# Performance work log

Hardware: AMD Instinct MI355X
Metric: run time of the kernel (lower is better)

The kernel has to match this reference:

```python
import jax, jax.numpy as jnp
import numpy as np

N_NODES = 50000
N_EDGES = 800000
IN_CH, HID_CH, OUT_CH = 128, 128, 64


def setup_inputs() -> dict:
    key = jax.random.key(0)
    k1, k2, k3, k4, k5, k6 = jax.random.split(key, 6)
    x = jax.random.normal(k1, (N_NODES, IN_CH), dtype=jnp.float32)
    edge_index = jax.random.randint(k2, (2, N_EDGES), 0, N_NODES, dtype=jnp.int64)
    # Glorot init like PyG GCNConv; bias zeros-like but random small for test coverage
    s1 = jnp.sqrt(6.0 / (IN_CH + HID_CH)).astype(jnp.float32)
    s2 = jnp.sqrt(6.0 / (HID_CH + OUT_CH)).astype(jnp.float32)
    W1 = jax.random.uniform(k3, (IN_CH, HID_CH), jnp.float32, -s1, s1)
    b1 = jax.random.normal(k4, (HID_CH,), jnp.float32) * 0.01
    W2 = jax.random.uniform(k5, (HID_CH, OUT_CH), jnp.float32, -s2, s2)
    b2 = jax.random.normal(k6, (OUT_CH,), jnp.float32) * 0.01
    return {"x": x, "edge_index": edge_index, "W1": W1, "b1": b1, "W2": W2, "b2": b2}


def gcn_conv(x, edge_index, W, b):
    """PyG GCNConv: add self-loops, symmetric D^-1/2 (A+I) D^-1/2 normalization,
    then aggregate linearly-transformed neighbor features + bias."""
    n = x.shape[0]
    h = x @ W  # [N, F_out]
    src, dst = edge_index[0], edge_index[1]
    # degree counts self-loop (weight 1) plus in-edges at dst
    deg = 1.0 + jax.ops.segment_sum(jnp.ones_like(src, dtype=h.dtype), dst, num_segments=n)
    dinv = jax.lax.rsqrt(deg)  # deg >= 1, no zeros
    norm = dinv[src] * dinv[dst]  # [E]
    agg = jax.ops.segment_sum(h[src] * norm[:, None], dst, num_segments=n)
    # self-loop contribution: norm = dinv[i]*dinv[i] = 1/deg[i]
    return agg + h * (1.0 / deg)[:, None] + b


def reference(x, edge_index, W1, b1, W2, b2):
    # eval-mode forward: dropout is identity
    h = gcn_conv(x, edge_index, W1, b1)
    h = jax.nn.relu(h)
    out = gcn_conv(h, edge_index, W2, b2)
    return out
```

## Files before the change

### kernel.cpp

```cpp
#include <hip/hip_runtime.h>
#include <hip/hip_fp16.h>


typedef _Float16 f16;
typedef __attribute__((ext_vector_type(8))) _Float16 f16x8;
typedef __attribute__((ext_vector_type(4))) float f32x4;

__global__ __launch_bounds__(256) void deg_prep_kernel(const int* __restrict__ dst,
                                                       int* __restrict__ deg,
                                                       int* __restrict__ posw,
                                                       const float* __restrict__ W1,
                                                       const float* __restrict__ W2,
                                                       f16* __restrict__ Wt1,
                                                       f16* __restrict__ Wt2, int E) {
    int gid = blockIdx.x * 256 + threadIdx.x;
    if (gid < E) posw[gid] = atomicAdd(&deg[dst[gid]], 1);
    if (gid < 128 * 128) {
        int k = gid >> 7, c = gid & 127;
        Wt1[c * 136 + k] = (f16)W1[gid];
    } else if (gid < 128 * 128 + 128 * 64) {
        int j = gid - 128 * 128;
        int k = j >> 6, c = j & 63;
        Wt2[c * 136 + k] = (f16)W2[j];
    }
}

__global__ __launch_bounds__(1024) void scan1_kernel(const int* __restrict__ deg,
                                                     int* __restrict__ rowptr,
                                                     int* __restrict__ bsum,
                                                     float* __restrict__ dinv, int N) {
    __shared__ int wsum[16];
    const int tid = threadIdx.x, lane = tid & 63, wid = tid >> 6;
    const int idx = blockIdx.x * 1024 + tid;
    int v = (idx < N) ? deg[idx] : 0;
    if (idx < N) dinv[idx] = rsqrtf((float)v + 1.0f);
    int incl = v;
#pragma unroll
    for (int off = 1; off < 64; off <<= 1) {
        int t = __shfl_up(incl, off, 64);
        if (lane >= off) incl += t;
    }
    if (lane == 63) wsum[wid] = incl;
    __syncthreads();
    if (wid == 0) {
        int s = (lane < 16) ? wsum[lane] : 0;
#pragma unroll
        for (int off = 1; off < 16; off <<= 1) {
            int t = __shfl_up(s, off, 64);
            if (lane >= off) s += t;
        }
        if (lane < 16) wsum[lane] = s;
    }
    __syncthreads();
    int waveoff = (wid == 0) ? 0 : wsum[wid - 1];
    if (idx < N) rowptr[idx] = waveoff + incl - v;
    if (tid == 1023) bsum[blockIdx.x] = waveoff + incl;
}

__global__ __launch_bounds__(1024) void scan23_kernel(int* __restrict__ rowptr,
                                                      const int* __restrict__ bsum,
                                                      int N, int nb) {
    __shared__ int pfx_s;
    const int tid = threadIdx.x;
    if (tid < 64) {
        int v = (tid < nb && tid < blockIdx.x) ? bsum[tid] : 0;
#pragma unroll
        for (int off = 32; off; off >>= 1) v += __shfl_xor(v, off, 64);
        if (tid == 0) pfx_s = v;
    }
    if (blockIdx.x == 0 && tid >= 64 && tid < 128) {
        int l = tid - 64;
        int v = (l < nb) ? bsum[l] : 0;
#pragma unroll
        for (int off = 32; off; off >>= 1) v += __shfl_xor(v, off, 64);
        if (l == 0) rowptr[N] = v;
    }
    __syncthreads();
    int idx = blockIdx.x * 1024 + tid;
    if (idx < N) rowptr[idx] += pfx_s;
}

template <int KOUT, bool F32IN>
__device__ __forceinline__ void gemm_body(int bid, const void* __restrict__ Xv,
                                          const f16* __restrict__ Wt,
                                          f16* __restrict__ H, int N, f16* Wl) {
    constexpr int CT = KOUT / 16;
    const int tid = threadIdx.x;
    constexpr int CHUNKS = KOUT * 136 / 8;
    {
        const uint4* s = (const uint4*)Wt;
        uint4* d = (uint4*)Wl;
        for (int i = tid; i < CHUNKS; i += 256) d[i] = s[i];
    }
    __syncthreads();

    const int lane = tid & 63, wid = tid >> 6;
    const int c = lane & 15, kseg = lane >> 4;
    const int row0 = bid * 64 + wid * 16;
    int arow = row0 + c;
    if (arow >= N) arow = N - 1;

    f32x4 acc[CT];
#pragma unroll
    for (int t = 0; t < CT; ++t) acc[t] = (f32x4){0.f, 0.f, 0.f, 0.f};

#pragma unroll
    for (int kt = 0; kt < 4; ++kt) {
        const int k0 = kt * 32;
        f16x8 a;
        if (F32IN) {
            const float* xp = (const float*)Xv + (long)arow * 128 + k0 + kseg * 8;
            float4 x0 = *(const float4*)xp;
            float4 x1 = *(const float4*)(xp + 4);
            a[0] = (f16)x0.x; a[1] = (f16)x0.y; a[2] = (f16)x0.z; a[3] = (f16)x0.w;
            a[4] = (f16)x1.x; a[5] = (f16)x1.y; a[6] = (f16)x1.z; a[7] = (f16)x1.w;
        } else {
            a = *(const f16x8*)((const f16*)Xv + (long)arow * 128 + k0 + kseg * 8);
        }
#pragma unroll
        for (int ct = 0; ct < CT; ++ct) {
            f16x8 b = *(const f16x8*)&Wl[(ct * 16 + c) * 136 + k0 + kseg * 8];
            acc[ct] = __builtin_amdgcn_mfma_f32_16x16x32_f16(a, b, acc[ct], 0, 0, 0);
        }
    }

    const int rbase = row0 + kseg * 4;
#pragma unroll
    for (int ct = 0; ct < CT; ++ct)
#pragma unroll
        for (int r = 0; r < 4; ++r) {
            int row = rbase + r;
            if (row < N) H[(long)row * KOUT + ct * 16 + c] = (f16)acc[ct][r];
        }
}

template <int KOUT, bool F32IN>
__global__ __launch_bounds__(256) void gemm_kernel(const void* __restrict__ Xv,
                                                   const f16* __restrict__ Wt,
                                                   f16* __restrict__ H, int N) {
    __shared__ f16 Wl[KOUT * 136];
    gemm_body<KOUT, F32IN>(blockIdx.x, Xv, Wt, H, N, Wl);
}

__global__ __launch_bounds__(256) void fill_gemm_kernel(const int* __restrict__ src,
                                                        const int* __restrict__ dst,
                                                        const int* __restrict__ posw,
                                                        const float* __restrict__ dinv,
                                                        const int* __restrict__ rowptr,
                                                        float2* __restrict__ pairs, int E,
                                                        const float* __restrict__ x,
                                                        const f16* __restrict__ Wt1,
                                                        f16* __restrict__ h1, int N, int GB) {
    __shared__ f16 Wl[128 * 136];
    if ((int)blockIdx.x < GB) {
        gemm_body<128, true>(blockIdx.x, x, Wt1, h1, N, Wl);
        return;
    }
    int e = (blockIdx.x - GB) * 256 + threadIdx.x;
    if (e >= E) return;
    int s = src[e], d = dst[e];
    float2 p;
    p.x = __int_as_float(s);
    p.y = dinv[s] * dinv[d];
    pairs[rowptr[d] + posw[e]] = p;
}

template <int F, bool RELU, bool OUTF16>
__global__ __launch_bounds__(256) void gather_kernel(const void* __restrict__ Hv,
                                                     const int* __restrict__ rowptr,
                                                     const float2* __restrict__ pairs,
                                                     const float* __restrict__ dinv,
                                                     const float* __restrict__ bias,
                                                     void* __restrict__ outv, int N) {
    const int wid = threadIdx.x >> 6;
    const int lane = threadIdx.x & 63;
    const int node = blockIdx.x * 4 + wid;
    if (node >= N) return;
    const int start = rowptr[node], end = rowptr[node + 1];
    const float4* pp4 = (const float4*)pairs;

    if (F == 128) {
        const __half2* Hu = (const __half2*)Hv;
        float ax = 0.f, ay = 0.f;
        int e = start;
        if ((e & 1) && e < end) {
            float2 p0 = pairs[e];
            float2 f0 = __half22float2(Hu[(long)__float_as_int(p0.x) * 64 + lane]);
            ax += f0.x * p0.y; ay += f0.y * p0.y;
            ++e;
        }
        for (; e + 15 < end; e += 16) {
            float4 q[8];
#pragma unroll
            for (int j = 0; j < 8; ++j) q[j] = pp4[(e >> 1) + j];
            __half2 uu[16];
#pragma unroll
            for (int j = 0; j < 8; ++j) {
                uu[2 * j]     = Hu[(long)__float_as_int(q[j].x) * 64 + lane];
                uu[2 * j + 1] = Hu[(long)__float_as_int(q[j].z) * 64 + lane];
            }
#pragma unroll
            for (int j = 0; j < 8; ++j) {
                float2 f0 = __half22float2(uu[2 * j]);
                float2 f1 = __half22float2(uu[2 * j + 1]);
                ax += f0.x * q[j].y + f1.x * q[j].w;
                ay += f0.y * q[j].y + f1.y * q[j].w;
            }
        }
        for (; e + 3 < end; e += 4) {
            float4 q0 = pp4[e >> 1], q1 = pp4[(e >> 1) + 1];
            __half2 u0 = Hu[(long)__float_as_int(q0.x) * 64 + lane];
            __half2 u1 = Hu[(long)__float_as_int(q0.z) * 64 + lane];
            __half2 u2 = Hu[(long)__float_as_int(q1.x) * 64 + lane];
            __half2 u3 = Hu[(long)__float_as_int(q1.z) * 64 + lane];
            float2 f0 = __half22float2(u0), f1 = __half22float2(u1);
            float2 f2 = __half22float2(u2), f3 = __half22float2(u3);
            ax += f0.x * q0.y + f1.x * q0.w + f2.x * q1.y + f3.x * q1.w;
            ay += f0.y * q0.y + f1.y * q0.w + f2.y * q1.y + f3.y * q1.w;
        }
        for (; e < end; ++e) {
            float2 p0 = pairs[e];
            float2 f0 = __half22float2(Hu[(long)__float_as_int(p0.x) * 64 + lane]);
            ax += f0.x * p0.y; ay += f0.y * p0.y;
        }
        float di = dinv[node];
        float d2 = di * di;
        float2 fs = __half22float2(Hu[(long)node * 64 + lane]);
        float2 bz = ((const float2*)bias)[lane];
        float zx = ax + fs.x * d2 + bz.x;
        float zy = ay + fs.y * d2 + bz.y;
        if (RELU) { zx = fmaxf(zx, 0.f); zy = fmaxf(zy, 0.f); }
        if (OUTF16) {
            ((__half2*)outv)[(long)node * 64 + lane] = __float22half2_rn(make_float2(zx, zy));
        } else {
            float2 o = {zx, zy};
            ((float2*)outv)[(long)node * 64 + lane] = o;
        }
    } else {
        const __half* Hh = (const __half*)Hv;
        float acc = 0.f;
        int e = start;
        if ((e & 1) && e < end) {
            float2 p0 = pairs[e];
            acc += __half2float(Hh[(long)__float_as_int(p0.x) * 64 + lane]) * p0.y;
            ++e;
        }
        for (; e + 15 < end; e += 16) {
            float4 q[8];
#pragma unroll
            for (int j = 0; j < 8; ++j) q[j] = pp4[(e >> 1) + j];
            __half uu[16];
#pragma unroll
            for (int j = 0; j < 8; ++j) {
                uu[2 * j]     = Hh[(long)__float_as_int(q[j].x) * 64 + lane];
                uu[2 * j + 1] = Hh[(long)__float_as_int(q[j].z) * 64 + lane];
            }
#pragma unroll
            for (int j = 0; j < 8; ++j)
                acc += __half2float(uu[2 * j]) * q[j].y + __half2float(uu[2 * j + 1]) * q[j].w;
        }
        for (; e + 3 < end; e += 4) {
            float4 q0 = pp4[e >> 1], q1 = pp4[(e >> 1) + 1];
            float h0 = __half2float(Hh[(long)__float_as_int(q0.x) * 64 + lane]);
            float h1 = __half2float(Hh[(long)__float_as_int(q0.z) * 64 + lane]);
            float h2 = __half2float(Hh[(long)__float_as_int(q1.x) * 64 + lane]);
            float h3 = __half2float(Hh[(long)__float_as_int(q1.z) * 64 + lane]);
            acc += h0 * q0.y + h1 * q0.w + h2 * q1.y + h3 * q1.w;
        }
        for (; e < end; ++e) {
            float2 p0 = pairs[e];
            acc += __half2float(Hh[(long)__float_as_int(p0.x) * 64 + lane]) * p0.y;
        }
        float di = dinv[node];
        float z = acc + __half2float(Hh[(long)node * 64 + lane]) * (di * di) + bias[lane];
        if (RELU) z = fmaxf(z, 0.f);
        ((float*)outv)[(long)node * 64 + lane] = z;
    }
}

extern "C" void kernel_launch(void* const* d_in, const int* in_sizes, int n_in,
                              void* d_out, int out_size, void* d_ws, size_t ws_size,
                              hipStream_t stream) {
    const float* x  = (const float*)d_in[0];
    const int*   ei = (const int*)d_in[1];
    const float* W1 = (const float*)d_in[2];
    const float* b1 = (const float*)d_in[3];
    const float* W2 = (const float*)d_in[4];
    const float* b2 = (const float*)d_in[5];
    float* out = (float*)d_out;

    const int N = in_sizes[0] / 128;
    const int E = in_sizes[1] / 2;
    const int* src = ei;
    const int* dst = ei + E;
    const int NB = (N + 1023) / 1024;

    float* ws = (float*)d_ws;
    float2* pairs = (float2*)ws;
    long off = 2L * E;
    int* posw   = (int*)(ws + off); off += E;
    int* deg    = (int*)(ws + off); off += N;
    int* rowptr = (int*)(ws + off); off += N + 1;
    int* bsum   = (int*)(ws + off); off += 64;
    float* dinv = ws + off;        off += N;
    off = (off + 3) & ~3L;
    f16* Wt1 = (f16*)(ws + off); off += (128 * 136) / 2;
    f16* Wt2 = (f16*)(ws + off); off += (64 * 136) / 2;
    f16* h1  = (f16*)(ws + off); off += (long)N * 64;
    f16* z1  = (f16*)(ws + off); off += (long)N * 64;
    f16* h2  = (f16*)(ws + off); off += (long)N * 32;

    hipMemsetAsync(deg, 0, (size_t)N * sizeof(int), stream);
    deg_prep_kernel<<<(E + 255) / 256, 256, 0, stream>>>(dst, deg, posw, W1, W2, Wt1, Wt2, E);
    scan1_kernel<<<NB, 1024, 0, stream>>>(deg, rowptr, bsum, dinv, N);
    scan23_kernel<<<NB, 1024, 0, stream>>>(rowptr, bsum, N, NB);

    const int GB = (N + 63) / 64;
    const int FB = (E + 255) / 256;
    fill_gemm_kernel<<<GB + FB, 256, 0, stream>>>(src, dst, posw, dinv, rowptr, pairs, E,
                                                  x, Wt1, h1, N, GB);

    gather_kernel<128, true, true><<<(N + 3) / 4, 256, 0, stream>>>(h1, rowptr, pairs, dinv, b1, z1, N);

    gemm_kernel<64, false><<<(N + 63) / 64, 256, 0, stream>>>(z1, Wt2, h2, N);
    gather_kernel<64, false, false><<<(N + 3) / 4, 256, 0, stream>>>(h2, rowptr, pairs, dinv, b2, out, N);
}
```

Before: 228.7 us.

## Fuse degree counting with first GEMM and split layer-1 gather into column halves

The separate weight-transpose pass is removed, and each GEMM block now converts the fp32 weights to transposed fp16 in shared memory itself. The degree atomics are fused into the first GEMM launch, so the GEMM runs before the scan instead of alongside the fill. Fill becomes its own kernel. The 128-wide first-layer gather is split into two launches, each covering 64 columns with one half per lane, which may improve cache locality of each pass but reads the CSR pairs twice and adds launches. Every GEMM block now redoes the weight conversion, which adds redundant work.

```diff
diff --git a/kernel.cpp b/kernel.cpp
--- a/kernel.cpp
+++ b/kernel.cpp
@@ -5,25 +5,6 @@
 typedef _Float16 f16;
 typedef __attribute__((ext_vector_type(8))) _Float16 f16x8;
 typedef __attribute__((ext_vector_type(4))) float f32x4;
-
-__global__ __launch_bounds__(256) void deg_prep_kernel(const int* __restrict__ dst,
-                                                       int* __restrict__ deg,
-                                                       int* __restrict__ posw,
-                                                       const float* __restrict__ W1,
-                                                       const float* __restrict__ W2,
-                                                       f16* __restrict__ Wt1,
-                                                       f16* __restrict__ Wt2, int E) {
-    int gid = blockIdx.x * 256 + threadIdx.x;
-    if (gid < E) posw[gid] = atomicAdd(&deg[dst[gid]], 1);
-    if (gid < 128 * 128) {
-        int k = gid >> 7, c = gid & 127;
-        Wt1[c * 136 + k] = (f16)W1[gid];
-    } else if (gid < 128 * 128 + 128 * 64) {
-        int j = gid - 128 * 128;
-        int k = j >> 6, c = j & 63;
-        Wt2[c * 136 + k] = (f16)W2[j];
-    }
-}
 
 __global__ __launch_bounds__(1024) void scan1_kernel(const int* __restrict__ deg,
                                                      int* __restrict__ rowptr,
@@ -80,17 +61,35 @@
     if (idx < N) rowptr[idx] += pfx_s;
 }
 
+__global__ __launch_bounds__(256) void fill_kernel(const int* __restrict__ src,
+                                                   const int* __restrict__ dst,
+                                                   const int* __restrict__ posw,
+                                                   const float* __restrict__ dinv,
+                                                   const int* __restrict__ rowptr,
+                                                   float2* __restrict__ pairs, int E) {
+    int e = blockIdx.x * 256 + threadIdx.x;
+    if (e >= E) return;
+    int s = src[e], d = dst[e];
+    float2 p;
+    p.x = __int_as_float(s);
+    p.y = dinv[s] * dinv[d];
+    pairs[rowptr[d] + posw[e]] = p;
+}
+
 template <int KOUT, bool F32IN>
 __device__ __forceinline__ void gemm_body(int bid, const void* __restrict__ Xv,
-                                          const f16* __restrict__ Wt,
+                                          const float* __restrict__ W,
                                           f16* __restrict__ H, int N, f16* Wl) {
     constexpr int CT = KOUT / 16;
     const int tid = threadIdx.x;
-    constexpr int CHUNKS = KOUT * 136 / 8;
-    {
-        const uint4* s = (const uint4*)Wt;
-        uint4* d = (uint4*)Wl;
-        for (int i = tid; i < CHUNKS; i += 256) d[i] = s[i];
+    for (int i4 = tid; i4 < 128 * KOUT / 4; i4 += 256) {
+        int flat = i4 * 4;
+        int k = flat / KOUT, c = flat % KOUT;
+        float4 w = *(const float4*)&W[flat];
+        Wl[(c + 0) * 136 + k] = (f16)w.x;
+        Wl[(c + 1) * 136 + k] = (f16)w.y;
+        Wl[(c + 2) * 136 + k] = (f16)w.z;
+        Wl[(c + 3) * 136 + k] = (f16)w.w;
     }
     __syncthreads();
 
@@ -136,37 +135,29 @@
 
 template <int KOUT, bool F32IN>
 __global__ __launch_bounds__(256) void gemm_kernel(const void* __restrict__ Xv,
-                                                   const f16* __restrict__ Wt,
+                                                   const float* __restrict__ W,
                                                    f16* __restrict__ H, int N) {
     __shared__ f16 Wl[KOUT * 136];
-    gemm_body<KOUT, F32IN>(blockIdx.x, Xv, Wt, H, N, Wl);
-}
-
-__global__ __launch_bounds__(256) void fill_gemm_kernel(const int* __restrict__ src,
-                                                        const int* __restrict__ dst,
-                                                        const int* __restrict__ posw,
-                                                        const float* __restrict__ dinv,
-                                                        const int* __restrict__ rowptr,
-                                                        float2* __restrict__ pairs, int E,
-                                                        const float* __restrict__ x,
-                                                        const f16* __restrict__ Wt1,
-                                                        f16* __restrict__ h1, int N, int GB) {
+    gemm_body<KOUT, F32IN>(blockIdx.x, Xv, W, H, N, Wl);
+}
+
+__global__ __launch_bounds__(256) void deg_gemm_kernel(const int* __restrict__ dst,
+                                                       int* __restrict__ deg,
+                                                       int* __restrict__ posw, int E,
+                                                       const float* __restrict__ x,
+                                                       const float* __restrict__ W1,
+                                                       f16* __restrict__ h1, int N, int GB) {
     __shared__ f16 Wl[128 * 136];
     if ((int)blockIdx.x < GB) {
-        gemm_body<128, true>(blockIdx.x, x, Wt1, h1, N, Wl);
+        gemm_body<128, true>(blockIdx.x, x, W1, h1, N, Wl);
         return;
     }
     int e = (blockIdx.x - GB) * 256 + threadIdx.x;
-    if (e >= E) return;
-    int s = src[e], d = dst[e];
-    float2 p;
-    p.x = __int_as_float(s);
-    p.y = dinv[s] * dinv[d];
-    pairs[rowptr[d] + posw[e]] = p;
-}
-
-template <int F, bool RELU, bool OUTF16>
-__global__ __launch_bounds__(256) void gather_kernel(const void* __restrict__ Hv,
+    if (e < E) posw[e] = atomicAdd(&deg[dst[e]], 1);
+}
+
+template <int STRIDE, int COLOFF, bool RELU, bool OUTF16>
+__global__ __launch_bounds__(256) void gather_kernel(const __half* __restrict__ H,
                                                      const int* __restrict__ rowptr,
                                                      const float2* __restrict__ pairs,
                                                      const float* __restrict__ dinv,
@@ -178,103 +169,48 @@
     if (node >= N) return;
     const int start = rowptr[node], end = rowptr[node + 1];
     const float4* pp4 = (const float4*)pairs;
-
-    if (F == 128) {
-        const __half2* Hu = (const __half2*)Hv;
-        float ax = 0.f, ay = 0.f;
-        int e = start;
-        if ((e & 1) && e < end) {
-            float2 p0 = pairs[e];
-            float2 f0 = __half22float2(Hu[(long)__float_as_int(p0.x) * 64 + lane]);
-            ax += f0.x * p0.y; ay += f0.y * p0.y;
-            ++e;
-        }
-        for (; e + 15 < end; e += 16) {
-            float4 q[8];
-#pragma unroll
-            for (int j = 0; j < 8; ++j) q[j] = pp4[(e >> 1) + j];
-            __half2 uu[16];
-#pragma unroll
-            for (int j = 0; j < 8; ++j) {
-                uu[2 * j]     = Hu[(long)__float_as_int(q[j].x) * 64 + lane];
-                uu[2 * j + 1] = Hu[(long)__float_as_int(q[j].z) * 64 + lane];
-            }
-#pragma unroll
-            for (int j = 0; j < 8; ++j) {
-                float2 f0 = __half22float2(uu[2 * j]);
-                float2 f1 = __half22float2(uu[2 * j + 1]);
-                ax += f0.x * q[j].y + f1.x * q[j].w;
-                ay += f0.y * q[j].y + f1.y * q[j].w;
-            }
-        }
-        for (; e + 3 < end; e += 4) {
-            float4 q0 = pp4[e >> 1], q1 = pp4[(e >> 1) + 1];
-            __half2 u0 = Hu[(long)__float_as_int(q0.x) * 64 + lane];
-            __half2 u1 = Hu[(long)__float_as_int(q0.z) * 64 + lane];
-            __half2 u2 = Hu[(long)__float_as_int(q1.x) * 64 + lane];
-            __half2 u3 = Hu[(long)__float_as_int(q1.z) * 64 + lane];
-            float2 f0 = __half22float2(u0), f1 = __half22float2(u1);
-            float2 f2 = __half22float2(u2), f3 = __half22float2(u3);
-            ax += f0.x * q0.y + f1.x * q0.w + f2.x * q1.y + f3.x * q1.w;
-            ay += f0.y * q0.y + f1.y * q0.w + f2.y * q1.y + f3.y * q1.w;
-        }
-        for (; e < end; ++e) {
-            float2 p0 = pairs[e];
-            float2 f0 = __half22float2(Hu[(long)__float_as_int(p0.x) * 64 + lane]);
-            ax += f0.x * p0.y; ay += f0.y * p0.y;
-        }
-        float di = dinv[node];
-        float d2 = di * di;
-        float2 fs = __half22float2(Hu[(long)node * 64 + lane]);
-        float2 bz = ((const float2*)bias)[lane];
-        float zx = ax + fs.x * d2 + bz.x;
-        float zy = ay + fs.y * d2 + bz.y;
-        if (RELU) { zx = fmaxf(zx, 0.f); zy = fmaxf(zy, 0.f); }
-        if (OUTF16) {
-            ((__half2*)outv)[(long)node * 64 + lane] = __float22half2_rn(make_float2(zx, zy));
-        } else {
-            float2 o = {zx, zy};
-            ((float2*)outv)[(long)node * 64 + lane] = o;
-        }
+    const __half* Hh = H + COLOFF + lane;
+
+    float acc = 0.f;
+    int e = start;
+    if ((e & 1) && e < end) {
+        float2 p0 = pairs[e];
+        acc += __half2float(Hh[(long)__float_as_int(p0.x) * STRIDE]) * p0.y;
+        ++e;
+    }
+    for (; e + 15 < end; e += 16) {
+        float4 q[8];
+#pragma unroll
+        for (int j = 0; j < 8; ++j) q[j] = pp4[(e >> 1) + j];
+        __half uu[16];
+#pragma unroll
+        for (int j = 0; j < 8; ++j) {
+            uu[2 * j]     = Hh[(long)__float_as_int(q[j].x) * STRIDE];
+            uu[2 * j + 1] = Hh[(long)__float_as_int(q[j].z) * STRIDE];
+        }
+#pragma unroll
+        for (int j = 0; j < 8; ++j)
+            acc += __half2float(uu[2 * j]) * q[j].y + __half2float(uu[2 * j + 1]) * q[j].w;
+    }
+    for (; e + 3 < end; e += 4) {
+        float4 q0 = pp4[e >> 1], q1 = pp4[(e >> 1) + 1];
+        float h0 = __half2float(Hh[(long)__float_as_int(q0.x) * STRIDE]);
+        float h1 = __half2float(Hh[(long)__float_as_int(q0.z) * STRIDE]);
+        float h2 = __half2float(Hh[(long)__float_as_int(q1.x) * STRIDE]);
+        float h3 = __half2float(Hh[(long)__float_as_int(q1.z) * STRIDE]);
+        acc += h0 * q0.y + h1 * q0.w + h2 * q1.y + h3 * q1.w;
+    }
+    for (; e < end; ++e) {
+        float2 p0 = pairs[e];
+        acc += __half2float(Hh[(long)__float_as_int(p0.x) * STRIDE]) * p0.y;
+    }
+    float di = dinv[node];
+    float z = acc + __half2float(Hh[(long)node * STRIDE]) * (di * di) + bias[COLOFF + lane];
+    if (RELU) z = fmaxf(z, 0.f);
+    if (OUTF16) {
+        ((__half*)outv)[(long)node * STRIDE + COLOFF + lane] = __float2half(z);
     } else {
-        const __half* Hh = (const __half*)Hv;
-        float acc = 0.f;
-        int e = start;
-        if ((e & 1) && e < end) {
-            float2 p0 = pairs[e];
-            acc += __half2float(Hh[(long)__float_as_int(p0.x) * 64 + lane]) * p0.y;
-            ++e;
-        }
-        for (; e + 15 < end; e += 16) {
-            float4 q[8];
-#pragma unroll
-            for (int j = 0; j < 8; ++j) q[j] = pp4[(e >> 1) + j];
-            __half uu[16];
-#pragma unroll
-            for (int j = 0; j < 8; ++j) {
-                uu[2 * j]     = Hh[(long)__float_as_int(q[j].x) * 64 + lane];
-                uu[2 * j + 1] = Hh[(long)__float_as_int(q[j].z) * 64 + lane];
-            }
-#pragma unroll
-            for (int j = 0; j < 8; ++j)
-                acc += __half2float(uu[2 * j]) * q[j].y + __half2float(uu[2 * j + 1]) * q[j].w;
-        }
-        for (; e + 3 < end; e += 4) {
-            float4 q0 = pp4[e >> 1], q1 = pp4[(e >> 1) + 1];
-            float h0 = __half2float(Hh[(long)__float_as_int(q0.x) * 64 + lane]);
-            float h1 = __half2float(Hh[(long)__float_as_int(q0.z) * 64 + lane]);
-            float h2 = __half2float(Hh[(long)__float_as_int(q1.x) * 64 + lane]);
-            float h3 = __half2float(Hh[(long)__float_as_int(q1.z) * 64 + lane]);
-            acc += h0 * q0.y + h1 * q0.w + h2 * q1.y + h3 * q1.w;
-        }
-        for (; e < end; ++e) {
-            float2 p0 = pairs[e];
-            acc += __half2float(Hh[(long)__float_as_int(p0.x) * 64 + lane]) * p0.y;
-        }
-        float di = dinv[node];
-        float z = acc + __half2float(Hh[(long)node * 64 + lane]) * (di * di) + bias[lane];
-        if (RELU) z = fmaxf(z, 0.f);
-        ((float*)outv)[(long)node * 64 + lane] = z;
+        ((float*)outv)[(long)node * STRIDE + COLOFF + lane] = z;
     }
 }
 
@@ -304,24 +240,25 @@
     int* bsum   = (int*)(ws + off); off += 64;
     float* dinv = ws + off;        off += N;
     off = (off + 3) & ~3L;
-    f16* Wt1 = (f16*)(ws + off); off += (128 * 136) / 2;
-    f16* Wt2 = (f16*)(ws + off); off += (64 * 136) / 2;
-    f16* h1  = (f16*)(ws + off); off += (long)N * 64;
-    f16* z1  = (f16*)(ws + off); off += (long)N * 64;
-    f16* h2  = (f16*)(ws + off); off += (long)N * 32;
+    f16* h1 = (f16*)(ws + off); off += (long)N * 64;
+    f16* z1 = (f16*)(ws + off); off += (long)N * 64;
+    f16* h2 = (f16*)(ws + off); off += (long)N * 32;
+
+    const int GB = (N + 63) / 64;
+    const int DB = (E + 255) / 256;
 
     hipMemsetAsync(deg, 0, (size_t)N * sizeof(int), stream);
-    deg_prep_kernel<<<(E + 255) / 256, 256, 0, stream>>>(dst, deg, posw, W1, W2, Wt1, Wt2, E);
+    deg_gemm_kernel<<<GB + DB, 256, 0, stream>>>(dst, deg, posw, E, x, W1, h1, N, GB);
     scan1_kernel<<<NB, 1024, 0, stream>>>(deg, rowptr, bsum, dinv, N);
     scan23_kernel<<<NB, 1024, 0, stream>>>(rowptr, bsum, N, NB);
-
-    const int GB = (N + 63) / 64;
-    const int FB = (E + 255) / 256;
-    fill_gemm_kernel<<<GB + FB, 256, 0, stream>>>(src, dst, posw, dinv, rowptr, pairs, E,
-                                                  x, Wt1, h1, N, GB);
-
-    gather_kernel<128, true, true><<<(N + 3) / 4, 256, 0, stream>>>(h1, rowptr, pairs, dinv, b1, z1, N);
-
-    gemm_kernel<64, false><<<(N + 63) / 64, 256, 0, stream>>>(z1, Wt2, h2, N);
-    gather_kernel<64, false, false><<<(N + 3) / 4, 256, 0, stream>>>(h2, rowptr, pairs, dinv, b2, out, N);
-}
+    fill_kernel<<<(E + 255) / 256, 256, 0, stream>>>(src, dst, posw, dinv, rowptr, pairs, E);
+
+    gather_kernel<128, 0, true, true><<<(N + 3) / 4, 256, 0, stream>>>(
+        (const __half*)h1, rowptr, pairs, dinv, b1, z1, N);
+    gather_kernel<128, 64, true, true><<<(N + 3) / 4, 256, 0, stream>>>(
+        (const __half*)h1, rowptr, pairs, dinv, b1, z1, N);
+
+    gemm_kernel<64, false><<<(N + 63) / 64, 256, 0, stream>>>(z1, W2, h2, N);
+    gather_kernel<64, 0, false, false><<<(N + 3) / 4, 256, 0, stream>>>(
+        (const __half*)h2, rowptr, pairs, dinv, b2, out, N);
+}
```

Result: slower. 253.1 us (+10.7%).

## Fuse layer-1 aggregation with per-node layer-2 GEMV and drop weight prep

Applied to the files above, without the earlier changes.

The layer-1 gather now also performs the ReLU and multiplies the node's hidden row by W2 in LDS. This removes the z1 intermediate buffer and the separate second GEMM launch. Weight transposition to fp16 moves into each GEMM and gather block, read straight from the fp32 weights, so the standalone weight-prep work is gone. The cost is that every 4-node gather block re-reads and transposes the whole 32KB W2 into LDS. That adds a large amount of redundant L2 traffic, LDS stores that may hit bank conflicts, and higher LDS use that can limit occupancy.

```diff
diff --git a/kernel.cpp b/kernel.cpp
--- a/kernel.cpp
+++ b/kernel.cpp
@@ -6,23 +6,11 @@
 typedef __attribute__((ext_vector_type(8))) _Float16 f16x8;
 typedef __attribute__((ext_vector_type(4))) float f32x4;
 
-__global__ __launch_bounds__(256) void deg_prep_kernel(const int* __restrict__ dst,
-                                                       int* __restrict__ deg,
-                                                       int* __restrict__ posw,
-                                                       const float* __restrict__ W1,
-                                                       const float* __restrict__ W2,
-                                                       f16* __restrict__ Wt1,
-                                                       f16* __restrict__ Wt2, int E) {
-    int gid = blockIdx.x * 256 + threadIdx.x;
-    if (gid < E) posw[gid] = atomicAdd(&deg[dst[gid]], 1);
-    if (gid < 128 * 128) {
-        int k = gid >> 7, c = gid & 127;
-        Wt1[c * 136 + k] = (f16)W1[gid];
-    } else if (gid < 128 * 128 + 128 * 64) {
-        int j = gid - 128 * 128;
-        int k = j >> 6, c = j & 63;
-        Wt2[c * 136 + k] = (f16)W2[j];
-    }
+__global__ __launch_bounds__(256) void deg_pos_kernel(const int* __restrict__ dst,
+                                                      int* __restrict__ deg,
+                                                      int* __restrict__ posw, int E) {
+    int e = blockIdx.x * 256 + threadIdx.x;
+    if (e < E) posw[e] = atomicAdd(&deg[dst[e]], 1);
 }
 
 __global__ __launch_bounds__(1024) void scan1_kernel(const int* __restrict__ deg,
@@ -82,15 +70,18 @@
 
 template <int KOUT, bool F32IN>
 __device__ __forceinline__ void gemm_body(int bid, const void* __restrict__ Xv,
-                                          const f16* __restrict__ Wt,
+                                          const float* __restrict__ W,
                                           f16* __restrict__ H, int N, f16* Wl) {
     constexpr int CT = KOUT / 16;
     const int tid = threadIdx.x;
-    constexpr int CHUNKS = KOUT * 136 / 8;
-    {
-        const uint4* s = (const uint4*)Wt;
-        uint4* d = (uint4*)Wl;
-        for (int i = tid; i < CHUNKS; i += 256) d[i] = s[i];
+    for (int i4 = tid; i4 < 128 * KOUT / 4; i4 += 256) {
+        int flat = i4 * 4;
+        int k = flat / KOUT, c = flat % KOUT;
+        float4 w = *(const float4*)&W[flat];
+        Wl[(c + 0) * 136 + k] = (f16)w.x;
+        Wl[(c + 1) * 136 + k] = (f16)w.y;
+        Wl[(c + 2) * 136 + k] = (f16)w.z;
+        Wl[(c + 3) * 136 + k] = (f16)w.w;
     }
     __syncthreads();
 
@@ -134,14 +125,6 @@
         }
 }
 
-template <int KOUT, bool F32IN>
-__global__ __launch_bounds__(256) void gemm_kernel(const void* __restrict__ Xv,
-                                                   const f16* __restrict__ Wt,
-                                                   f16* __restrict__ H, int N) {
-    __shared__ f16 Wl[KOUT * 136];
-    gemm_body<KOUT, F32IN>(blockIdx.x, Xv, Wt, H, N, Wl);
-}
-
 __global__ __launch_bounds__(256) void fill_gemm_kernel(const int* __restrict__ src,
                                                         const int* __restrict__ dst,
                                                         const int* __restrict__ posw,
@@ -149,11 +132,11 @@
                                                         const int* __restrict__ rowptr,
                                                         float2* __restrict__ pairs, int E,
                                                         const float* __restrict__ x,
-                                                        const f16* __restrict__ Wt1,
+                                                        const float* __restrict__ W1,
                                                         f16* __restrict__ h1, int N, int GB) {
     __shared__ f16 Wl[128 * 136];
     if ((int)blockIdx.x < GB) {
-        gemm_body<128, true>(blockIdx.x, x, Wt1, h1, N, Wl);
+        gemm_body<128, true>(blockIdx.x, x, W1, h1, N, Wl);
         return;
     }
     int e = (blockIdx.x - GB) * 256 + threadIdx.x;
@@ -165,13 +148,103 @@
     pairs[rowptr[d] + posw[e]] = p;
 }
 
-template <int F, bool RELU, bool OUTF16>
-__global__ __launch_bounds__(256) void gather_kernel(const void* __restrict__ Hv,
-                                                     const int* __restrict__ rowptr,
-                                                     const float2* __restrict__ pairs,
-                                                     const float* __restrict__ dinv,
-                                                     const float* __restrict__ bias,
-                                                     void* __restrict__ outv, int N) {
+__global__ __launch_bounds__(256) void gather_gemv_kernel(const __half* __restrict__ H,
+                                                          const int* __restrict__ rowptr,
+                                                          const float2* __restrict__ pairs,
+                                                          const float* __restrict__ dinv,
+                                                          const float* __restrict__ b1,
+                                                          const float* __restrict__ W2,
+                                                          f16* __restrict__ h2, int N) {
+    __shared__ f16 W2t[64][130];
+    __shared__ __half z_lds[4][128];
+
+    const int tid = threadIdx.x;
+    for (int i = tid; i < 128 * 64 / 2; i += 256) {
+        int flat = i * 2;
+        int k = flat >> 6, c = flat & 63;
+        float2 w = *(const float2*)&W2[flat];
+        W2t[c][k] = (f16)w.x;
+        W2t[c + 1][k] = (f16)w.y;
+    }
+    __syncthreads();
+
+    const int wid = tid >> 6;
+    const int lane = tid & 63;
+    const int node = blockIdx.x * 4 + wid;
+    if (node >= N) return;
+    const int start = rowptr[node], end = rowptr[node + 1];
+    const float4* pp4 = (const float4*)pairs;
+    const __half2* Hu = (const __half2*)H;
+
+    float ax = 0.f, ay = 0.f;
+    int e = start;
+    if ((e & 1) && e < end) {
+        float2 p0 = pairs[e];
+        float2 f0 = __half22float2(Hu[(long)__float_as_int(p0.x) * 64 + lane]);
+        ax += f0.x * p0.y; ay += f0.y * p0.y;
+        ++e;
+    }
+    for (; e + 15 < end; e += 16) {
+        float4 q[8];
+#pragma unroll
+        for (int j = 0; j < 8; ++j) q[j] = pp4[(e >> 1) + j];
+        __half2 uu[16];
+#pragma unroll
+        for (int j = 0; j < 8; ++j) {
+            uu[2 * j]     = Hu[(long)__float_as_int(q[j].x) * 64 + lane];
+            uu[2 * j + 1] = Hu[(long)__float_as_int(q[j].z) * 64 + lane];
+        }
+#pragma unroll
+        for (int j = 0; j < 8; ++j) {
+            float2 f0 = __half22float2(uu[2 * j]);
+            float2 f1 = __half22float2(uu[2 * j + 1]);
+            ax += f0.x * q[j].y + f1.x * q[j].w;
+            ay += f0.y * q[j].y + f1.y * q[j].w;
+        }
+    }
+    for (; e + 3 < end; e += 4) {
+        float4 q0 = pp4[e >> 1], q1 = pp4[(e >> 1) + 1];
+        __half2 u0 = Hu[(long)__float_as_int(q0.x) * 64 + lane];
+        __half2 u1 = Hu[(long)__float_as_int(q0.z) * 64 + lane];
+        __half2 u2 = Hu[(long)__float_as_int(q1.x) * 64 + lane];
+        __half2 u3 = Hu[(long)__float_as_int(q1.z) * 64 + lane];
+        float2 f0 = __half22float2(u0), f1 = __half22float2(u1);
+        float2 f2 = __half22float2(u2), f3 = __half22float2(u3);
+        ax += f0.x * q0.y + f1.x * q0.w + f2.x * q1.y + f3.x * q1.w;
+        ay += f0.y * q0.y + f1.y * q0.w + f2.y * q1.y + f3.y * q1.w;
+    }
+    for (; e < end; ++e) {
+        float2 p0 = pairs[e];
+        float2 f0 = __half22float2(Hu[(long)__float_as_int(p0.x) * 64 + lane]);
+        ax += f0.x * p0.y; ay += f0.y * p0.y;
+    }
+    float di = dinv[node];
+    float d2 = di * di;
+    float2 fs = __half22float2(Hu[(long)node * 64 + lane]);
+    float2 bz = ((const float2*)b1)[lane];
+    float zx = fmaxf(ax + fs.x * d2 + bz.x, 0.f);
+    float zy = fmaxf(ay + fs.y * d2 + bz.y, 0.f);
+
+    *(__half2*)&z_lds[wid][2 * lane] = __float22half2_rn(make_float2(zx, zy));
+
+    const __half2* zrow = (const __half2*)&z_lds[wid][0];
+    const __half2* wrow = (const __half2*)&W2t[lane][0];
+    float acc = 0.f;
+#pragma unroll 8
+    for (int k2 = 0; k2 < 64; ++k2) {
+        float2 z2 = __half22float2(zrow[k2]);
+        float2 w2 = __half22float2(wrow[k2]);
+        acc += z2.x * w2.x + z2.y * w2.y;
+    }
+    h2[(long)node * 64 + lane] = (f16)acc;
+}
+
+__global__ __launch_bounds__(256) void gather64_kernel(const __half* __restrict__ H,
+                                                       const int* __restrict__ rowptr,
+                                                       const float2* __restrict__ pairs,
+                                                       const float* __restrict__ dinv,
+                                                       const float* __restrict__ bias,
+                                                       float* __restrict__ out, int N) {
     const int wid = threadIdx.x >> 6;
     const int lane = threadIdx.x & 63;
     const int node = blockIdx.x * 4 + wid;
@@ -179,103 +252,42 @@
     const int start = rowptr[node], end = rowptr[node + 1];
     const float4* pp4 = (const float4*)pairs;
 
-    if (F == 128) {
-        const __half2* Hu = (const __half2*)Hv;
-        float ax = 0.f, ay = 0.f;
-        int e = start;
-        if ((e & 1) && e < end) {
-            float2 p0 = pairs[e];
-            float2 f0 = __half22float2(Hu[(long)__float_as_int(p0.x) * 64 + lane]);
-            ax += f0.x * p0.y; ay += f0.y * p0.y;
-            ++e;
-        }
-        for (; e + 15 < end; e += 16) {
-            float4 q[8];
-#pragma unroll
-            for (int j = 0; j < 8; ++j) q[j] = pp4[(e >> 1) + j];
-            __half2 uu[16];
-#pragma unroll
-            for (int j = 0; j < 8; ++j) {
-                uu[2 * j]     = Hu[(long)__float_as_int(q[j].x) * 64 + lane];
-                uu[2 * j + 1] = Hu[(long)__float_as_int(q[j].z) * 64 + lane];
-            }
-#pragma unroll
-            for (int j = 0; j < 8; ++j) {
-                float2 f0 = __half22float2(uu[2 * j]);
-                float2 f1 = __half22float2(uu[2 * j + 1]);
-                ax += f0.x * q[j].y + f1.x * q[j].w;
-                ay += f0.y * q[j].y + f1.y * q[j].w;
-            }
-        }
-        for (; e + 3 < end; e += 4) {
-            float4 q0 = pp4[e >> 1], q1 = pp4[(e >> 1) + 1];
-            __half2 u0 = Hu[(long)__float_as_int(q0.x) * 64 + lane];
-            __half2 u1 = Hu[(long)__float_as_int(q0.z) * 64 + lane];
-            __half2 u2 = Hu[(long)__float_as_int(q1.x) * 64 + lane];
-            __half2 u3 = Hu[(long)__float_as_int(q1.z) * 64 + lane];
-            float2 f0 = __half22float2(u0), f1 = __half22float2(u1);
-            float2 f2 = __half22float2(u2), f3 = __half22float2(u3);
-            ax += f0.x * q0.y + f1.x * q0.w + f2.x * q1.y + f3.x * q1.w;
-            ay += f0.y * q0.y + f1.y * q0.w + f2.y * q1.y + f3.y * q1.w;
-        }
-        for (; e < end; ++e) {
-            float2 p0 = pairs[e];
-            float2 f0 = __half22float2(Hu[(long)__float_as_int(p0.x) * 64 + lane]);
-            ax += f0.x * p0.y; ay += f0.y * p0.y;
-        }
-        float di = dinv[node];
-        float d2 = di * di;
-        float2 fs = __half22float2(Hu[(long)node * 64 + lane]);
-        float2 bz = ((const float2*)bias)[lane];
-        float zx = ax + fs.x * d2 + bz.x;
-        float zy = ay + fs.y * d2 + bz.y;
-        if (RELU) { zx = fmaxf(zx, 0.f); zy = fmaxf(zy, 0.f); }
-        if (OUTF16) {
-            ((__half2*)outv)[(long)node * 64 + lane] = __float22half2_rn(make_float2(zx, zy));
-        } else {
-            float2 o = {zx, zy};
-            ((float2*)outv)[(long)node * 64 + lane] = o;
-        }
-    } else {
-        const __half* Hh = (const __half*)Hv;
-        float acc = 0.f;
-        int e = start;
-        if ((e & 1) && e < end) {
-            float2 p0 = pairs[e];
-            acc += __half2float(Hh[(long)__float_as_int(p0.x) * 64 + lane]) * p0.y;
-            ++e;
-        }
-        for (; e + 15 < end; e += 16) {
-            float4 q[8];
-#pragma unroll
-            for (int j = 0; j < 8; ++j) q[j] = pp4[(e >> 1) + j];
-            __half uu[16];
-#pragma unroll
-            for (int j = 0; j < 8; ++j) {
-                uu[2 * j]     = Hh[(long)__float_as_int(q[j].x) * 64 + lane];
-                uu[2 * j + 1] = Hh[(long)__float_as_int(q[j].z) * 64 + lane];
-            }
-#pragma unroll
-            for (int j = 0; j < 8; ++j)
-                acc += __half2float(uu[2 * j]) * q[j].y + __half2float(uu[2 * j + 1]) * q[j].w;
-        }
-        for (; e + 3 < end; e += 4) {
-            float4 q0 = pp4[e >> 1], q1 = pp4[(e >> 1) + 1];
-            float h0 = __half2float(Hh[(long)__float_as_int(q0.x) * 64 + lane]);
-            float h1 = __half2float(Hh[(long)__float_as_int(q0.z) * 64 + lane]);
-            float h2 = __half2float(Hh[(long)__float_as_int(q1.x) * 64 + lane]);
-            float h3 = __half2float(Hh[(long)__float_as_int(q1.z) * 64 + lane]);
-            acc += h0 * q0.y + h1 * q0.w + h2 * q1.y + h3 * q1.w;
-        }
-        for (; e < end; ++e) {
-            float2 p0 = pairs[e];
-            acc += __half2float(Hh[(long)__float_as_int(p0.x) * 64 + lane]) * p0.y;
-        }
-        float di = dinv[node];
-        float z = acc + __half2float(Hh[(long)node * 64 + lane]) * (di * di) + bias[lane];
-        if (RELU) z = fmaxf(z, 0.f);
-        ((float*)outv)[(long)node * 64 + lane] = z;
-    }
+    float acc = 0.f;
+    int e = start;
+    if ((e & 1) && e < end) {
+        float2 p0 = pairs[e];
+        acc += __half2float(H[(long)__float_as_int(p0.x) * 64 + lane]) * p0.y;
+        ++e;
+    }
+    for (; e + 15 < end; e += 16) {
+        float4 q[8];
+#pragma unroll
+        for (int j = 0; j < 8; ++j) q[j] = pp4[(e >> 1) + j];
+        __half uu[16];
+#pragma unroll
+        for (int j = 0; j < 8; ++j) {
+            uu[2 * j]     = H[(long)__float_as_int(q[j].x) * 64 + lane];
+            uu[2 * j + 1] = H[(long)__float_as_int(q[j].z) * 64 + lane];
+        }
+#pragma unroll
+        for (int j = 0; j < 8; ++j)
+            acc += __half2float(uu[2 * j]) * q[j].y + __half2float(uu[2 * j + 1]) * q[j].w;
+    }
+    for (; e + 3 < end; e += 4) {
+        float4 q0 = pp4[e >> 1], q1 = pp4[(e >> 1) + 1];
+        float h0 = __half2float(H[(long)__float_as_int(q0.x) * 64 + lane]);
+        float h1 = __half2float(H[(long)__float_as_int(q0.z) * 64 + lane]);
+        float h2 = __half2float(H[(long)__float_as_int(q1.x) * 64 + lane]);
+        float h3 = __half2float(H[(long)__float_as_int(q1.z) * 64 + lane]);
+        acc += h0 * q0.y + h1 * q0.w + h2 * q1.y + h3 * q1.w;
+    }
+    for (; e < end; ++e) {
+        float2 p0 = pairs[e];
+        acc += __half2float(H[(long)__float_as_int(p0.x) * 64 + lane]) * p0.y;
+    }
+    float di = dinv[node];
+    float z = acc + __half2float(H[(long)node * 64 + lane]) * (di * di) + bias[lane];
+    out[(long)node * 64 + lane] = z;
 }
 
 extern "C" void kernel_launch(void* const* d_in, const int* in_sizes, int n_in,
@@ -304,24 +316,23 @@
     int* bsum   = (int*)(ws + off); off += 64;
     float* dinv = ws + off;        off += N;
     off = (off + 3) & ~3L;
-    f16* Wt1 = (f16*)(ws + off); off += (128 * 136) / 2;
-    f16* Wt2 = (f16*)(ws + off); off += (64 * 136) / 2;
-    f16* h1  = (f16*)(ws + off); off += (long)N * 64;
-    f16* z1  = (f16*)(ws + off); off += (long)N * 64;
-    f16* h2  = (f16*)(ws + off); off += (long)N * 32;
+    f16* h1 = (f16*)(ws + off); off += (long)N * 64;
+    f16* h2 = (f16*)(ws + off); off += (long)N * 32;
+
+    const int GB = (N + 63) / 64;
+    const int FB = (E + 255) / 256;
 
     hipMemsetAsync(deg, 0, (size_t)N * sizeof(int), stream);
-    deg_prep_kernel<<<(E + 255) / 256, 256, 0, stream>>>(dst, deg, posw, W1, W2, Wt1, Wt2, E);
+    deg_pos_kernel<<<FB, 256, 0, stream>>>(dst, deg, posw, E);
     scan1_kernel<<<NB, 1024, 0, stream>>>(deg, rowptr, bsum, dinv, N);
     scan23_kernel<<<NB, 1024, 0, stream>>>(rowptr, bsum, N, NB);
 
-    const int GB = (N + 63) / 64;
-    const int FB = (E + 255) / 256;
     fill_gemm_kernel<<<GB + FB, 256, 0, stream>>>(src, dst, posw, dinv, rowptr, pairs, E,
-                                                  x, Wt1, h1, N, GB);
-
-    gather_kernel<128, true, true><<<(N + 3) / 4, 256, 0, stream>>>(h1, rowptr, pairs, dinv, b1, z1, N);
-
-    gemm_kernel<64, false><<<(N + 63) / 64, 256, 0, stream>>>(z1, Wt2, h2, N);
-    gather_kernel<64, false, false><<<(N + 3) / 4, 256, 0, stream>>>(h2, rowptr, pairs, dinv, b2, out, N);
-}
+                                                  x, W1, h1, N, GB);
+
+    gather_gemv_kernel<<<(N + 3) / 4, 256, 0, stream>>>(
+        (const __half*)h1, rowptr, pairs, dinv, b1, W2, h2, N);
+
+    gather64_kernel<<<(N + 3) / 4, 256, 0, stream>>>(
+        (const __half*)h2, rowptr, pairs, dinv, b2, out, N);
+}
```

New measurement: 259.1 us. +13.3%, slower.
